# Kernel tuning notes

Hardware: AMD Instinct MI355X
Metric: run time of the kernel (lower is better)

Reference implementation:

```python
import jax, jax.numpy as jnp
import numpy as np

B, F, I, E, K, G, S = 2, 768, 1536, 8, 5, 8, 1024
ALPHA = 0.02  # leaky relu slope


def setup_inputs() -> dict:
    key = jax.random.key(0)
    ks = jax.random.split(key, 6)
    return {
        "x": jax.random.normal(ks[0], (B, F, S), jnp.float32),
        "w0_gate": jax.random.normal(ks[1], (F, E), jnp.float32) * 0.02,
        "w0": jax.random.normal(ks[2], (E, F, 3 * I), jnp.float32) * 0.02,
        "w1": jax.random.normal(ks[3], (K, I // G, 3 * I), jnp.float32) * 0.02,
        "w2_gate": jax.random.normal(ks[4], (I, E), jnp.float32) * 0.02,
        "w2": jax.random.normal(ks[5], (E, I, F), jnp.float32) * 0.02,
    }


def _rmsnorm(x):
    # feature-wise normalization (interpretation of tf.norm in source), axis=1 is channel dim
    return x * jax.lax.rsqrt(jnp.mean(jnp.square(x), axis=1, keepdims=True) + 1e-6)


def _leaky(x):
    return jax.nn.leaky_relu(x, ALPHA)


def _moe(inp, w_gate, w):
    # inp: [B, C, S], w_gate: [C, E], w: [E, C, O]; top-1 routing w/ straight-through gates
    logits = jnp.einsum('bcs,ce->bes', inp, w_gate)                  # 1x1 conv gate
    gates = jax.nn.softmax(logits, axis=1)
    one_hot = jax.nn.one_hot(jnp.argmax(logits, axis=1), logits.shape[1], axis=1)  # [B,E,S]
    st = one_hot - jax.lax.stop_gradient(gates) + gates              # straight-through
    # dense-equivalent of gather -> per-expert GEMM -> scatter
    out = jnp.einsum('bes,bcs,eco->bos', one_hot * st, inp, w)       # [B, O, S]
    loss = jnp.sum(jnp.mean(gates, axis=(0, 2)) * jnp.mean(one_hot, axis=(0, 2)))
    return loss, out


def _causal_grouped_conv(x, w, groups):
    # x: [B, C, S], w: [K, C//groups, O] (keras Conv1D kernel layout)
    k = w.shape[0]
    x = jnp.pad(x, ((0, 0), (0, 0), (k - 1, 0)))                     # causal left pad
    kernel = jnp.transpose(w, (2, 1, 0))                             # [O, C//g, K]
    return jax.lax.conv_general_dilated(
        x, kernel, window_strides=(1,), padding='VALID',
        dimension_numbers=('NCH', 'OIH', 'NCH'), feature_group_count=groups)


def reference(x, w0_gate, w0, w1, w2_gate, w2):
    seq = x.shape[2]
    divisor = (jnp.arange(seq, dtype=x.dtype) + 1.0).reshape(1, 1, -1)
    # input MoE: F -> 3*I
    loss0, h = _moe(x, w0_gate, w0)
    depth, scale, shift = jnp.split(h, 3, axis=1)                    # each [B, I, S]
    cum = jnp.cumsum(depth, axis=-1)                                 # linear-attention cumsum
    h = _leaky(_rmsnorm(cum / (divisor * scale + shift)))
    # grouped causal conv I -> 3*I
    h = _causal_grouped_conv(h, w1, G)
    s0, s1, sh = jnp.split(h, 3, axis=1)
    h = _leaky(_rmsnorm(s0 * s1 + sh))                               # split_norm
    # output MoE: I -> F
    loss1, out = _moe(h, w2_gate, w2)
    init_scale = jnp.asarray(1.0, x.dtype)
    return out * init_scale, loss0 + loss1
```

## Files before the change

### kernel.cpp

```cpp
#include <hip/hip_runtime.h>
#include <hip/hip_bf16.h>
#include <cstdint>
#include <cstddef>

#define ALPHA 0.02f
static constexpr int B_ = 2, F_ = 768, I_ = 1536, E_ = 8, S_ = 1024;
static constexpr int O3I = 3 * I_;
static constexpr int NTOK = B_ * S_;

__device__ __forceinline__ float waveSum(float v) {
  #pragma unroll
  for (int off = 32; off; off >>= 1) v += __shfl_xor(v, off);
  return v;
}
__device__ __forceinline__ double waveSumD(double v) {
  #pragma unroll
  for (int off = 32; off; off >>= 1) v += __shfl_xor(v, off);
  return v;
}

__global__ __launch_bounds__(64) void zero_meta(float* gs0, float* gs2, int* cnt0, int* cnt2) {
  int i = threadIdx.x;
  if (i < 8) { gs0[i] = 0.f; gs2[i] = 0.f; cnt0[i] = 0; cnt2[i] = 0; }
}

__global__ __launch_bounds__(256) void gate0_kernel(const float* __restrict__ x, const float* __restrict__ wg,
                                                    float* __restrict__ gs, int* __restrict__ cnt,
                                                    int* __restrict__ bucket) {
  const int tk = threadIdx.x & 63;
  const int cpart = threadIdx.x >> 6;
  const int t = blockIdx.x * 64 + tk;
  const int b = t >> 10, s = t & 1023;
  double l[8] = {0,0,0,0,0,0,0,0};
  const float* xb = x + (size_t)b * F_ * S_ + s;
  for (int c = cpart * 192; c < cpart * 192 + 192; ++c) {
    double xv = (double)xb[(size_t)c * S_];
    const float* w = wg + c * 8;
    #pragma unroll
    for (int e = 0; e < 8; ++e) l[e] += xv * (double)w[e];
  }
  __shared__ double red[4][8][64];
  #pragma unroll
  for (int e = 0; e < 8; ++e) red[cpart][e][tk] = l[e];
  __syncthreads();
  if (cpart == 0) {
    double lg[8]; double m = -1e300; int am = 0;
    #pragma unroll
    for (int e = 0; e < 8; ++e) {
      lg[e] = red[0][e][tk] + red[1][e][tk] + red[2][e][tk] + red[3][e][tk];
      if (lg[e] > m) { m = lg[e]; am = e; }
    }
    float den = 0.f;
    #pragma unroll
    for (int e = 0; e < 8; ++e) den += expf((float)(lg[e] - m));
    float inv = 1.f / den;
    #pragma unroll
    for (int e = 0; e < 8; ++e) atomicAdd(&gs[e], expf((float)(lg[e] - m)) * inv);
    int slot = atomicAdd(&cnt[am], 1);
    bucket[am * NTOK + slot] = t;
  }
}

__global__ __launch_bounds__(256) void gate2_kernel(const float* __restrict__ hb, const float* __restrict__ wg,
                                                    float* __restrict__ gs, int* __restrict__ cnt,
                                                    int* __restrict__ bucket) {
  const int t = blockIdx.x;
  const float* p = hb + (size_t)t * I_;
  double l[8] = {0,0,0,0,0,0,0,0};
  #pragma unroll
  for (int r = 0; r < 6; ++r) {
    int i = threadIdx.x + r * 256;
    double xv = (double)p[i];
    const float* w = wg + i * 8;
    #pragma unroll
    for (int e = 0; e < 8; ++e) l[e] += xv * (double)w[e];
  }
  __shared__ double red[8][4];
  #pragma unroll
  for (int e = 0; e < 8; ++e) {
    double v = waveSumD(l[e]);
    if ((threadIdx.x & 63) == 0) red[e][threadIdx.x >> 6] = v;
  }
  __syncthreads();
  if (threadIdx.x == 0) {
    double lg[8]; double m = -1e300; int am = 0;
    #pragma unroll
    for (int e = 0; e < 8; ++e) {
      lg[e] = red[e][0] + red[e][1] + red[e][2] + red[e][3];
      if (lg[e] > m) { m = lg[e]; am = e; }
    }
    float den = 0.f;
    #pragma unroll
    for (int e = 0; e < 8; ++e) den += expf((float)(lg[e] - m));
    float inv = 1.f / den;
    #pragma unroll
    for (int e = 0; e < 8; ++e) atomicAdd(&gs[e], expf((float)(lg[e] - m)) * inv);
    int slot = atomicAdd(&cnt[am], 1);
    bucket[am * NTOK + slot] = t;
  }
}

template<int C, int O, bool IN_TM, bool OUT_TM, bool DACC>
__global__ __launch_bounds__(256) void moe_gemm(const float* __restrict__ inp, const float* __restrict__ w,
                                                const int* __restrict__ cnt, const int* __restrict__ bucket,
                                                float* __restrict__ out) {
  using AccT = typename std::conditional<DACC, double, float>::type;
  const int e = blockIdx.y;
  const int n = cnt[e];
  const int t0 = blockIdx.z * 64;
  if (t0 >= n) return;
  const int ob = blockIdx.x * 128;
  const int tid = threadIdx.x;
  const int o_t = tid & 15;
  const int t_t = tid >> 4;
  __shared__ float xs[16][64];
  __shared__ float wsh[16][128];
  __shared__ int toks[64];
  __shared__ int bases[64];
  if (tid < 64) {
    int idx = t0 + tid;
    int tt = (idx < n) ? bucket[e * NTOK + idx] : -1;
    toks[tid] = tt;
    if (tt >= 0) {
      int b = tt >> 10, s = tt & 1023;
      bases[tid] = IN_TM ? tt * C : b * C * S_ + s;
    } else bases[tid] = -1;
  }
  __syncthreads();
  AccT acc[4][8];
  #pragma unroll
  for (int i = 0; i < 4; ++i)
    #pragma unroll
    for (int j = 0; j < 8; ++j) acc[i][j] = (AccT)0;
  const float* wE = w + (size_t)e * C * O + ob;
  for (int c0 = 0; c0 < C; c0 += 16) {
    #pragma unroll
    for (int r = 0; r < 4; ++r) {
      int idx = r * 256 + tid;
      int cc = idx >> 6, tk = idx & 63;
      int bs = bases[tk];
      xs[cc][tk] = (bs >= 0) ? inp[(size_t)bs + (size_t)(c0 + cc) * (IN_TM ? 1 : S_)] : 0.f;
    }
    #pragma unroll
    for (int r = 0; r < 8; ++r) {
      int idx = r * 256 + tid;
      int cc = idx >> 7, oo = idx & 127;
      wsh[cc][oo] = wE[(size_t)(c0 + cc) * O + oo];
    }
    __syncthreads();
    #pragma unroll
    for (int cc = 0; cc < 16; ++cc) {
      float4 av = *reinterpret_cast<const float4*>(&xs[cc][t_t * 4]);
      float4 b0 = *reinterpret_cast<const float4*>(&wsh[cc][o_t * 8]);
      float4 b1 = *reinterpret_cast<const float4*>(&wsh[cc][o_t * 8 + 4]);
      AccT a[4] = {(AccT)av.x, (AccT)av.y, (AccT)av.z, (AccT)av.w};
      AccT bv[8] = {(AccT)b0.x, (AccT)b0.y, (AccT)b0.z, (AccT)b0.w,
                    (AccT)b1.x, (AccT)b1.y, (AccT)b1.z, (AccT)b1.w};
      #pragma unroll
      for (int i = 0; i < 4; ++i)
        #pragma unroll
        for (int j = 0; j < 8; ++j) acc[i][j] += a[i] * bv[j];
    }
    __syncthreads();
  }
  #pragma unroll
  for (int i = 0; i < 4; ++i) {
    int tk = t_t * 4 + i;
    int tt = toks[tk];
    if (tt < 0) continue;
    if (OUT_TM) {
      float* op = out + (size_t)tt * O + ob + o_t * 8;
      float4 v0 = {(float)acc[i][0], (float)acc[i][1], (float)acc[i][2], (float)acc[i][3]};
      float4 v1 = {(float)acc[i][4], (float)acc[i][5], (float)acc[i][6], (float)acc[i][7]};
      *reinterpret_cast<float4*>(op) = v0;
      *reinterpret_cast<float4*>(op + 4) = v1;
    } else {
      int b = tt >> 10, s = tt & 1023;
      #pragma unroll
      for (int j = 0; j < 8; ++j)
        out[((size_t)b * O + ob + o_t * 8 + j) * S_ + s] = (float)acc[i][j];
    }
  }
}

__global__ __launch_bounds__(256) void cumsum_partial(const float* __restrict__ h0, float* __restrict__ part) {
  const int i = blockIdx.x * 256 + threadIdx.x;
  const int chunk = blockIdx.y, b = blockIdx.z;
  float sum = 0.f;
  const float* base = h0 + ((size_t)(b * S_ + chunk * 128)) * O3I + i;
  for (int s = 0; s < 128; ++s) sum += base[(size_t)s * O3I];
  part[((size_t)(b * 8 + chunk)) * I_ + i] = sum;
}

__global__ __launch_bounds__(256) void cumsum_scan(float* part) {
  const int idx = blockIdx.x * 256 + threadIdx.x;
  const int b = idx / 1536, i = idx - b * 1536;
  float run = 0.f;
  #pragma unroll
  for (int c = 0; c < 8; ++c) {
    size_t p = ((size_t)(b * 8 + c)) * I_ + i;
    float v = part[p]; part[p] = run; run += v;
  }
}

__global__ __launch_bounds__(256) void cumsum_apply(const float* __restrict__ h0, const float* __restrict__ part,
                                                    float* __restrict__ y) {
  const int i = blockIdx.x * 256 + threadIdx.x;
  const int chunk = blockIdx.y, b = blockIdx.z;
  float run = part[((size_t)(b * 8 + chunk)) * I_ + i];
  for (int s = chunk * 128; s < chunk * 128 + 128; ++s) {
    const float* row = h0 + ((size_t)(b * S_ + s)) * O3I;
    run += row[i];
    double d = (double)(s + 1) * (double)row[I_ + i] + (double)row[2 * I_ + i];
    y[((size_t)(b * S_ + s)) * I_ + i] = (float)((double)run / d);
  }
}

__global__ __launch_bounds__(256) void rmsnorm_leaky_kernel(float* __restrict__ buf) {
  const int t = blockIdx.x;
  float* p = buf + (size_t)t * I_;
  float v[6]; float ssum = 0.f;
  #pragma unroll
  for (int r = 0; r < 6; ++r) { v[r] = p[threadIdx.x + r * 256]; ssum += v[r] * v[r]; }
  ssum = waveSum(ssum);
  __shared__ float red[4];
  if ((threadIdx.x & 63) == 0) red[threadIdx.x >> 6] = ssum;
  __syncthreads();
  float tot = red[0] + red[1] + red[2] + red[3];
  float rs = rsqrtf(tot * (1.f / I_) + 1e-6f);
  #pragma unroll
  for (int r = 0; r < 6; ++r) {
    float y = v[r] * rs;
    p[threadIdx.x + r * 256] = y > 0.f ? y : ALPHA * y;
  }
}

__global__ __launch_bounds__(256) void split_norm_kernel(const float* __restrict__ hc, float* __restrict__ hb) {
  const int t = blockIdx.x;
  const float* p = hc + (size_t)t * O3I;
  float z[6]; float ssum = 0.f;
  #pragma unroll
  for (int r = 0; r < 6; ++r) {
    int i = threadIdx.x + r * 256;
    float zz = p[i] * p[I_ + i] + p[2 * I_ + i];
    z[r] = zz; ssum += zz * zz;
  }
  ssum = waveSum(ssum);
  __shared__ float red[4];
  if ((threadIdx.x & 63) == 0) red[threadIdx.x >> 6] = ssum;
  __syncthreads();
  float tot = red[0] + red[1] + red[2] + red[3];
  float rs = rsqrtf(tot * (1.f / I_) + 1e-6f);
  #pragma unroll
  for (int r = 0; r < 6; ++r) {
    float y = z[r] * rs;
    hb[(size_t)t * I_ + threadIdx.x + r * 256] = y > 0.f ? y : ALPHA * y;
  }
}

__global__ __launch_bounds__(256) void conv_kernel(const float* __restrict__ xin, const float* __restrict__ w1,
                                                   float* __restrict__ out) {
  const int bs = blockIdx.x;
  const int b = bs >> 5;
  const int s0 = (bs & 31) * 32;
  const int ob = blockIdx.y * 64;
  const int g = ob / 576;
  const int tid = threadIdx.x;
  const int ss = tid >> 6;
  const int ol = tid & 63;
  const int o = ob + ol;
  __shared__ float xl[192][40];
  for (int idx = tid; idx < 36 * 192; idx += 256) {
    int sl = idx / 192, ci = idx % 192;
    int s = s0 - 4 + sl;
    xl[ci][sl] = (s >= 0) ? xin[((size_t)(b * S_ + s)) * I_ + g * 192 + ci] : 0.f;
  }
  __syncthreads();
  float acc[8] = {0.f,0.f,0.f,0.f,0.f,0.f,0.f,0.f};
  const float* wb = w1 + o;
  for (int ci = 0; ci < 192; ++ci) {
    const float4* xr = reinterpret_cast<const float4*>(&xl[ci][ss * 8]);
    float4 v0 = xr[0], v1 = xr[1], v2 = xr[2];
    float xw[12] = {v0.x, v0.y, v0.z, v0.w, v1.x, v1.y, v1.z, v1.w, v2.x, v2.y, v2.z, v2.w};
    #pragma unroll
    for (int k = 0; k < 5; ++k) {
      float wv = wb[(size_t)(k * 192 + ci) * O3I];
      #pragma unroll
      for (int j = 0; j < 8; ++j) acc[j] += xw[j + k] * wv;
    }
  }
  float* op = out + ((size_t)(b * S_ + s0 + ss * 8)) * O3I + o;
  #pragma unroll
  for (int j = 0; j < 8; ++j) op[(size_t)j * O3I] = acc[j];
}

__global__ void finalize_loss(const float* gs0, const int* cnt0, const float* gs2, const int* cnt2,
                              float* outp) {
  float l = 0.f;
  for (int e = 0; e < 8; ++e) l += gs0[e] * (float)cnt0[e] + gs2[e] * (float)cnt2[e];
  *outp = l * (1.f / ((float)NTOK * (float)NTOK));
}

extern "C" void kernel_launch(void* const* d_in, const int* in_sizes, int n_in,
                              void* d_out, int out_size, void* d_ws, size_t ws_size,
                              hipStream_t stream) {
  const float* x   = (const float*)d_in[0];
  const float* w0g = (const float*)d_in[1];
  const float* w0  = (const float*)d_in[2];
  const float* w1  = (const float*)d_in[3];
  const float* w2g = (const float*)d_in[4];
  const float* w2  = (const float*)d_in[5];
  float* out = (float*)d_out;

  char* ws = (char*)d_ws;
  float* bufA    = (float*)ws;
  float* bufB    = (float*)(ws + 37748736);
  float* part    = (float*)(ws + 50331648);
  float* gs0     = (float*)(ws + 50429952);
  float* gs2     = (float*)(ws + 50429952 + 32);
  int*   cnt0    = (int*)(ws + 50430016);
  int*   cnt2    = (int*)(ws + 50430048);
  int*   bucket0 = (int*)(ws + 50430080);
  int*   bucket2 = (int*)(ws + 50495616);

  zero_meta<<<1, 64, 0, stream>>>(gs0, gs2, cnt0, cnt2);
  gate0_kernel<<<32, 256, 0, stream>>>(x, w0g, gs0, cnt0, bucket0);
  moe_gemm<F_, O3I, false, true, true><<<dim3(36, 8, 32), 256, 0, stream>>>(x, w0, cnt0, bucket0, bufA);
  cumsum_partial<<<dim3(6, 8, 2), 256, 0, stream>>>(bufA, part);
  cumsum_scan<<<12, 256, 0, stream>>>(part);
  cumsum_apply<<<dim3(6, 8, 2), 256, 0, stream>>>(bufA, part, bufB);
  rmsnorm_leaky_kernel<<<NTOK, 256, 0, stream>>>(bufB);
  conv_kernel<<<dim3(64, 72), 256, 0, stream>>>(bufB, w1, bufA);
  split_norm_kernel<<<NTOK, 256, 0, stream>>>(bufA, bufB);
  gate2_kernel<<<NTOK, 256, 0, stream>>>(bufB, w2g, gs2, cnt2, bucket2);
  moe_gemm<I_, F_, true, false, false><<<dim3(6, 8, 32), 256, 0, stream>>>(bufB, w2, cnt2, bucket2, out);
  finalize_loss<<<1, 1, 0, stream>>>(gs0, cnt0, gs2, cnt2, out + (size_t)B_ * F_ * S_);
}
```

Baseline: 1.515 ms.

## Use float accumulation for depth columns and widen cumsum chunking

```diff
diff --git a/kernel.cpp b/kernel.cpp
--- a/kernel.cpp
+++ b/kernel.cpp
@@ -2,11 +2,14 @@
 #include <hip/hip_bf16.h>
 #include <cstdint>
 #include <cstddef>
+#include <type_traits>
 
 #define ALPHA 0.02f
 static constexpr int B_ = 2, F_ = 768, I_ = 1536, E_ = 8, S_ = 1024;
 static constexpr int O3I = 3 * I_;
 static constexpr int NTOK = B_ * S_;
+static constexpr int NCH = 32;
+static constexpr int CHS = S_ / NCH;
 
 __device__ __forceinline__ float waveSum(float v) {
   #pragma unroll
@@ -103,13 +106,13 @@
 template<int C, int O, bool IN_TM, bool OUT_TM, bool DACC>
 __global__ __launch_bounds__(256) void moe_gemm(const float* __restrict__ inp, const float* __restrict__ w,
                                                 const int* __restrict__ cnt, const int* __restrict__ bucket,
-                                                float* __restrict__ out) {
+                                                float* __restrict__ out, int obase) {
   using AccT = typename std::conditional<DACC, double, float>::type;
   const int e = blockIdx.y;
   const int n = cnt[e];
   const int t0 = blockIdx.z * 64;
   if (t0 >= n) return;
-  const int ob = blockIdx.x * 128;
+  const int ob = obase + blockIdx.x * 128;
   const int tid = threadIdx.x;
   const int o_t = tid & 15;
   const int t_t = tid >> 4;
@@ -151,8 +154,8 @@
     #pragma unroll
     for (int cc = 0; cc < 16; ++cc) {
       float4 av = *reinterpret_cast<const float4*>(&xs[cc][t_t * 4]);
-      float4 b0 = *reinterpret_cast<const float4*>(&wsh[cc][o_t * 8]);
-      float4 b1 = *reinterpret_cast<const float4*>(&wsh[cc][o_t * 8 + 4]);
+      float4 b0 = *reinterpret_cast<const float4*>(&wsh[cc][o_t * 4]);
+      float4 b1 = *reinterpret_cast<const float4*>(&wsh[cc][64 + o_t * 4]);
       AccT a[4] = {(AccT)av.x, (AccT)av.y, (AccT)av.z, (AccT)av.w};
       AccT bv[8] = {(AccT)b0.x, (AccT)b0.y, (AccT)b0.z, (AccT)b0.w,
                     (AccT)b1.x, (AccT)b1.y, (AccT)b1.z, (AccT)b1.w};
@@ -169,16 +172,18 @@
     int tt = toks[tk];
     if (tt < 0) continue;
     if (OUT_TM) {
-      float* op = out + (size_t)tt * O + ob + o_t * 8;
+      float* op = out + (size_t)tt * O + ob;
       float4 v0 = {(float)acc[i][0], (float)acc[i][1], (float)acc[i][2], (float)acc[i][3]};
       float4 v1 = {(float)acc[i][4], (float)acc[i][5], (float)acc[i][6], (float)acc[i][7]};
-      *reinterpret_cast<float4*>(op) = v0;
-      *reinterpret_cast<float4*>(op + 4) = v1;
+      *reinterpret_cast<float4*>(op + o_t * 4) = v0;
+      *reinterpret_cast<float4*>(op + 64 + o_t * 4) = v1;
     } else {
       int b = tt >> 10, s = tt & 1023;
       #pragma unroll
-      for (int j = 0; j < 8; ++j)
-        out[((size_t)b * O + ob + o_t * 8 + j) * S_ + s] = (float)acc[i][j];
+      for (int j = 0; j < 4; ++j) {
+        out[((size_t)b * O + ob + o_t * 4 + j) * S_ + s] = (float)acc[i][j];
+        out[((size_t)b * O + ob + 64 + o_t * 4 + j) * S_ + s] = (float)acc[i][4 + j];
+      }
     }
   }
 }
@@ -187,9 +192,9 @@
   const int i = blockIdx.x * 256 + threadIdx.x;
   const int chunk = blockIdx.y, b = blockIdx.z;
   float sum = 0.f;
-  const float* base = h0 + ((size_t)(b * S_ + chunk * 128)) * O3I + i;
-  for (int s = 0; s < 128; ++s) sum += base[(size_t)s * O3I];
-  part[((size_t)(b * 8 + chunk)) * I_ + i] = sum;
+  const float* base = h0 + ((size_t)(b * S_ + chunk * CHS)) * O3I + i;
+  for (int s = 0; s < CHS; ++s) sum += base[(size_t)s * O3I];
+  part[((size_t)(b * NCH + chunk)) * I_ + i] = sum;
 }
 
 __global__ __launch_bounds__(256) void cumsum_scan(float* part) {
@@ -197,8 +202,8 @@
   const int b = idx / 1536, i = idx - b * 1536;
   float run = 0.f;
   #pragma unroll
-  for (int c = 0; c < 8; ++c) {
-    size_t p = ((size_t)(b * 8 + c)) * I_ + i;
+  for (int c = 0; c < NCH; ++c) {
+    size_t p = ((size_t)(b * NCH + c)) * I_ + i;
     float v = part[p]; part[p] = run; run += v;
   }
 }
@@ -207,8 +212,8 @@
                                                     float* __restrict__ y) {
   const int i = blockIdx.x * 256 + threadIdx.x;
   const int chunk = blockIdx.y, b = blockIdx.z;
-  float run = part[((size_t)(b * 8 + chunk)) * I_ + i];
-  for (int s = chunk * 128; s < chunk * 128 + 128; ++s) {
+  float run = part[((size_t)(b * NCH + chunk)) * I_ + i];
+  for (int s = chunk * CHS; s < chunk * CHS + CHS; ++s) {
     const float* row = h0 + ((size_t)(b * S_ + s)) * O3I;
     run += row[i];
     double d = (double)(s + 1) * (double)row[I_ + i] + (double)row[2 * I_ + i];
@@ -316,23 +321,24 @@
   float* bufA    = (float*)ws;
   float* bufB    = (float*)(ws + 37748736);
   float* part    = (float*)(ws + 50331648);
-  float* gs0     = (float*)(ws + 50429952);
-  float* gs2     = (float*)(ws + 50429952 + 32);
-  int*   cnt0    = (int*)(ws + 50430016);
-  int*   cnt2    = (int*)(ws + 50430048);
-  int*   bucket0 = (int*)(ws + 50430080);
-  int*   bucket2 = (int*)(ws + 50495616);
+  float* gs0     = (float*)(ws + 50724864);
+  float* gs2     = (float*)(ws + 50724896);
+  int*   cnt0    = (int*)(ws + 50724928);
+  int*   cnt2    = (int*)(ws + 50724960);
+  int*   bucket0 = (int*)(ws + 50724992);
+  int*   bucket2 = (int*)(ws + 50790528);
 
   zero_meta<<<1, 64, 0, stream>>>(gs0, gs2, cnt0, cnt2);
   gate0_kernel<<<32, 256, 0, stream>>>(x, w0g, gs0, cnt0, bucket0);
-  moe_gemm<F_, O3I, false, true, true><<<dim3(36, 8, 32), 256, 0, stream>>>(x, w0, cnt0, bucket0, bufA);
-  cumsum_partial<<<dim3(6, 8, 2), 256, 0, stream>>>(bufA, part);
+  moe_gemm<F_, O3I, false, true, false><<<dim3(12, 8, 32), 256, 0, stream>>>(x, w0, cnt0, bucket0, bufA, 0);
+  moe_gemm<F_, O3I, false, true, true><<<dim3(24, 8, 32), 256, 0, stream>>>(x, w0, cnt0, bucket0, bufA, I_);
+  cumsum_partial<<<dim3(6, NCH, 2), 256, 0, stream>>>(bufA, part);
   cumsum_scan<<<12, 256, 0, stream>>>(part);
-  cumsum_apply<<<dim3(6, 8, 2), 256, 0, stream>>>(bufA, part, bufB);
+  cumsum_apply<<<dim3(6, NCH, 2), 256, 0, stream>>>(bufA, part, bufB);
   rmsnorm_leaky_kernel<<<NTOK, 256, 0, stream>>>(bufB);
   conv_kernel<<<dim3(64, 72), 256, 0, stream>>>(bufB, w1, bufA);
   split_norm_kernel<<<NTOK, 256, 0, stream>>>(bufA, bufB);
   gate2_kernel<<<NTOK, 256, 0, stream>>>(bufB, w2g, gs2, cnt2, bucket2);
-  moe_gemm<I_, F_, true, false, false><<<dim3(6, 8, 32), 256, 0, stream>>>(bufB, w2, cnt2, bucket2, out);
+  moe_gemm<I_, F_, true, false, false><<<dim3(6, 8, 32), 256, 0, stream>>>(bufB, w2, cnt2, bucket2, out, 0);
   finalize_loss<<<1, 1, 0, stream>>>(gs0, cnt0, gs2, cnt2, out + (size_t)B_ * F_ * S_);
 }
```

New measurement: 1.555 ms. +2.6%, slower.
